# Optimization experiments

Hardware: AMD Instinct MI355X
Metric: run time of the kernel (lower is better)

The kernel has to match this reference:

```python
import jax, jax.numpy as jnp
import numpy as np

D_MODEL = 1024
H = 16
HEAD = D_MODEL // H  # 64


def setup_inputs() -> dict:
    key = jax.random.key(0)
    ks = jax.random.split(key, 10)
    B, S = 2, 2048
    x = jax.random.normal(ks[0], (B, S, D_MODEL), dtype=jnp.float32)
    y = jax.random.normal(ks[1], (B, S, D_MODEL), dtype=jnp.float32)
    mask = jnp.ones((B, S, S), dtype=jnp.float32)
    s = 1.0 / np.sqrt(D_MODEL)
    Wq = jax.random.normal(ks[2], (D_MODEL, D_MODEL), dtype=jnp.float32) * s
    Wk = jax.random.normal(ks[3], (D_MODEL, D_MODEL), dtype=jnp.float32) * s
    Wv = jax.random.normal(ks[4], (D_MODEL, D_MODEL), dtype=jnp.float32) * s
    Wo = jax.random.normal(ks[5], (D_MODEL, D_MODEL), dtype=jnp.float32) * s
    bq = jnp.zeros((D_MODEL,), jnp.float32)
    bk = jnp.zeros((D_MODEL,), jnp.float32)
    bv = jnp.zeros((D_MODEL,), jnp.float32)
    bo = jnp.zeros((D_MODEL,), jnp.float32)
    return {"x": x, "y": y, "mask": mask, "Wq": Wq, "bq": bq, "Wk": Wk,
            "bk": bk, "Wv": Wv, "bv": bv, "Wo": Wo, "bo": bo}


def reference(x, y, mask, Wq, bq, Wk, bk, Wv, bv, Wo, bo):
    # torch Linear: out = in @ W.T + b; here W stored as [out, in]
    B, Sq, D = x.shape
    Skv = y.shape[1]
    q = x @ Wq.T + bq  # [B, Sq, D]
    k = y @ Wk.T + bk  # [B, Skv, D]
    v = y @ Wv.T + bv
    # chunk(h, dim=-1) + cat(dim=0) == split feature dim into heads (head-major)
    q = q.reshape(B, Sq, H, HEAD)
    k = k.reshape(B, Skv, H, HEAD)
    v = v.reshape(B, Skv, H, HEAD)
    score = jnp.einsum('bqhd,bkhd->bhqk', q, k) / np.sqrt(HEAD)
    score = score + (1.0 - mask[:, None, :, :]) * -1e9
    attn = jax.nn.softmax(score, axis=-1)
    out = jnp.einsum('bhqk,bkhd->bqhd', attn, v).reshape(B, Sq, D)
    return out @ Wo.T + bo
```

## Files before the change

kernel.cpp:

```cpp
#include <hip/hip_runtime.h>
#include <hip/hip_bf16.h>
#include <cstdint>
#include <cstddef>

typedef __bf16 bf16x8 __attribute__((ext_vector_type(8)));
typedef float f32x4 __attribute__((ext_vector_type(4)));
typedef unsigned short u16;
typedef unsigned short u16x8 __attribute__((ext_vector_type(8)));
typedef unsigned int u32;

typedef __attribute__((address_space(1))) void gvoid_t;
typedef __attribute__((address_space(3))) void lvoid_t;

__device__ __forceinline__ void gld_lds16(const void* g, void* l) {
  __builtin_amdgcn_global_load_lds((gvoid_t*)g, (lvoid_t*)l, 16, 0, 0);
}

__device__ __forceinline__ u16 f2bf(float f) {
  u32 u = __float_as_uint(f);
  u += 0x7fffu + ((u >> 16) & 1u);
  return (u16)(u >> 16);
}
__device__ __forceinline__ u32 pack2(float a, float b) {
  __hip_bfloat162 h = __float22bfloat162_rn(float2{a, b});
  u32 r;
  __builtin_memcpy(&r, &h, 4);
  return r;
}
__device__ __forceinline__ bf16x8 ld_frag(const u16* p) {
  return __builtin_bit_cast(bf16x8, *(const uint4*)p);
}
__device__ __forceinline__ f32x4 mfma16(bf16x8 a, bf16x8 b, f32x4 c) {
  return __builtin_amdgcn_mfma_f32_16x16x32_bf16(a, b, c, 0, 0, 0);
}
__device__ __forceinline__ float ex2(float x) {
  return __builtin_amdgcn_exp2f(x);
}

#define D_MODEL 1024
#define SEQ     2048
#define NHEAD   16
#define QSC     0.1803368801f
#define MBIAS   (-1.4426950408e9f)

__global__ __launch_bounds__(256) void cvt_kernel(
    const float* __restrict__ x,  const float* __restrict__ y,
    const float* __restrict__ wq, const float* __restrict__ wk,
    const float* __restrict__ wv,
    u16* __restrict__ xb, u16* __restrict__ yb,
    u16* __restrict__ wqb, u16* __restrict__ wkb, u16* __restrict__ wvb) {
  const int t = blockIdx.y;
  const float* src;
  u16* dst;
  int n;
  float sc = 1.0f;
  if (t == 0)      { src = x;  dst = xb;  n = 4096 * 1024; }
  else if (t == 1) { src = y;  dst = yb;  n = 4096 * 1024; }
  else if (t == 2) { src = wq; dst = wqb; n = 1024 * 1024; sc = QSC; }
  else if (t == 3) { src = wk; dst = wkb; n = 1024 * 1024; }
  else             { src = wv; dst = wvb; n = 1024 * 1024; }
  const int i = (blockIdx.x * 256 + threadIdx.x) * 8;
  if (i >= n) return;
  const float4 a = *(const float4*)(src + i);
  const float4 b = *(const float4*)(src + i + 4);
  ushort4 lo, hi;
  lo.x = f2bf(a.x * sc); lo.y = f2bf(a.y * sc); lo.z = f2bf(a.z * sc); lo.w = f2bf(a.w * sc);
  hi.x = f2bf(b.x * sc); hi.y = f2bf(b.y * sc); hi.z = f2bf(b.z * sc); hi.w = f2bf(b.w * sc);
  *(ushort4*)(dst + i) = lo;
  *(ushort4*)(dst + i + 4) = hi;
}

__global__ __launch_bounds__(256) void prep_kernel(
    const float* __restrict__ mask, const float* __restrict__ wo,
    u16* __restrict__ biasC, u16* __restrict__ wob) {
  const int bid = blockIdx.x;
  if (bid < 4096) {
    const int i = (bid * 256 + threadIdx.x) * 8;
    const float4 a = *(const float4*)(mask + i);
    const float4 b = *(const float4*)(mask + i + 4);
    ushort4 lo, hi;
    lo.x = f2bf(MBIAS - a.x * MBIAS); lo.y = f2bf(MBIAS - a.y * MBIAS);
    lo.z = f2bf(MBIAS - a.z * MBIAS); lo.w = f2bf(MBIAS - a.w * MBIAS);
    hi.x = f2bf(MBIAS - b.x * MBIAS); hi.y = f2bf(MBIAS - b.y * MBIAS);
    hi.z = f2bf(MBIAS - b.z * MBIAS); hi.w = f2bf(MBIAS - b.w * MBIAS);
    *(ushort4*)(biasC + i) = lo;
    *(ushort4*)(biasC + i + 4) = hi;
  } else {
    const int i = ((bid - 4096) * 256 + threadIdx.x) * 8;
    const float4 a = *(const float4*)(wo + i);
    const float4 b = *(const float4*)(wo + i + 4);
    ushort4 lo, hi;
    lo.x = f2bf(a.x); lo.y = f2bf(a.y); lo.z = f2bf(a.z); lo.w = f2bf(a.w);
    hi.x = f2bf(b.x); hi.y = f2bf(b.y); hi.z = f2bf(b.z); hi.w = f2bf(b.w);
    *(ushort4*)(wob + i) = lo;
    *(ushort4*)(wob + i + 4) = hi;
  }
}

template <int MODE, typename OT>
__device__ __forceinline__ void gemm_block_128(const u16* __restrict__ A,
                                               const u16* __restrict__ W,
                                               const float* __restrict__ bias,
                                               float bscale,
                                               OT* __restrict__ D,
                                               int mb, int nb) {
  __shared__ __align__(16) u16 S[16384];
  u16* Asl = S;
  u16* Bsl = S + 8192;
  const int tid = threadIdx.x;
  const int w = tid >> 6, lane = tid & 63, quad = lane >> 4, l16 = lane & 15;
  const int wm = (w & 1) * 64, wn = (w >> 1) * 64;
  const int cidx = w * 64 + lane;

  f32x4 acc[4][4];
#pragma unroll
  for (int i = 0; i < 4; ++i)
#pragma unroll
    for (int j = 0; j < 4; ++j) acc[i][j] = f32x4{0.f, 0.f, 0.f, 0.f};

  for (int k0 = 0; k0 < 1024; k0 += 64) {
    __syncthreads();
#pragma unroll
    for (int t = 0; t < 4; ++t) {
      const int idx = t * 256 + cidx;
      const int row = idx >> 3;
      const int g = (idx & 7) ^ (row & 7);
      const size_t dst = (size_t)(t * 4 + w) * 1024;
      gld_lds16(A + (size_t)(mb * 128 + row) * 1024 + k0 + g * 8, (char*)Asl + dst);
      gld_lds16(W + (size_t)(nb * 128 + row) * 1024 + k0 + g * 8, (char*)Bsl + dst);
    }
    __syncthreads();

#pragma unroll
    for (int kk = 0; kk < 2; ++kk) {
      bf16x8 af[4], bfr[4];
#pragma unroll
      for (int i = 0; i < 4; ++i) {
        const int ar = wm + i * 16 + l16;
        const int br = wn + i * 16 + l16;
        af[i]  = ld_frag(Asl + ar * 64 + (((kk * 4 + quad) ^ (ar & 7)) * 8));
        bfr[i] = ld_frag(Bsl + br * 64 + (((kk * 4 + quad) ^ (br & 7)) * 8));
      }
#pragma unroll
      for (int i = 0; i < 4; ++i)
#pragma unroll
        for (int j = 0; j < 4; ++j) acc[i][j] = mfma16(af[i], bfr[j], acc[i][j]);
    }
  }

  if constexpr (MODE == 2) {
    __syncthreads();
#pragma unroll
    for (int i = 0; i < 4; ++i)
#pragma unroll
      for (int j = 0; j < 4; ++j) {
        const int dl = wn + j * 16 + l16;
        const float bv = bias[nb * 128 + dl];
        const int sx = (wm + i * 16 + quad * 4) ^ ((dl & 15) << 3);
        uint2 pv;
        pv.x = (u32)f2bf(acc[i][j][0] + bv) | ((u32)f2bf(acc[i][j][1] + bv) << 16);
        pv.y = (u32)f2bf(acc[i][j][2] + bv) | ((u32)f2bf(acc[i][j][3] + bv) << 16);
        *(uint2*)(S + dl * 128 + sx) = pv;
      }
    __syncthreads();
    const int dl = tid >> 1, half = tid & 1;
    const int bb = mb >> 4, s0 = (mb & 15) * 128;
    u16* vrow = (u16*)D + (size_t)(bb * 1024 + nb * 128 + dl) * SEQ + s0 + half * 64;
#pragma unroll
    for (int c = 0; c < 8; ++c) {
      const int pc = (half * 8 + c) ^ (dl & 15);
      *(uint4*)(vrow + c * 8) = *(const uint4*)(S + dl * 128 + pc * 8);
    }
  } else {
#pragma unroll
    for (int i = 0; i < 4; ++i)
#pragma unroll
      for (int j = 0; j < 4; ++j) {
        const int gn = nb * 128 + wn + j * 16 + l16;
        const float bv = bias[gn] * bscale;
#pragma unroll
        for (int r = 0; r < 4; ++r) {
          const int gm = mb * 128 + wm + i * 16 + quad * 4 + r;
          const float v = acc[i][j][r] + bv;
          if constexpr (sizeof(OT) == 2)
            D[(size_t)gm * 1024 + gn] = (OT)f2bf(v);
          else
            D[(size_t)gm * 1024 + gn] = (OT)v;
        }
      }
  }
}

__global__ __launch_bounds__(256) void qkv_kernel(
    const u16* __restrict__ xb, const u16* __restrict__ yb,
    const u16* __restrict__ Wqb, const u16* __restrict__ Wkb, const u16* __restrict__ Wvb,
    const float* __restrict__ bq, const float* __restrict__ bk, const float* __restrict__ bv,
    u16* __restrict__ qb, u16* __restrict__ kb, u16* __restrict__ vt) {
  const int mat = blockIdx.y >> 3;
  const int nb = blockIdx.y & 7;
  const int mb = blockIdx.x;
  if (mat == 0)      gemm_block_128<0, u16>(xb, Wqb, bq, QSC,  qb, mb, nb);
  else if (mat == 1) gemm_block_128<0, u16>(yb, Wkb, bk, 1.0f, kb, mb, nb);
  else               gemm_block_128<2, u16>(yb, Wvb, bv, 1.0f, vt, mb, nb);
}

__global__ __launch_bounds__(256) void oproj_kernel(
    const u16* __restrict__ ctx, const u16* __restrict__ Wob,
    const float* __restrict__ bo, float* __restrict__ out) {
  gemm_block_128<1, float>(ctx, Wob, bo, 1.0f, out, blockIdx.x, blockIdx.y);
}

__global__ __launch_bounds__(256) void attn_kernel(
    const u16* __restrict__ qb, const u16* __restrict__ kb,
    const u16* __restrict__ vt, const u16* __restrict__ biasC,
    u16* __restrict__ ctx) {
  const int h = blockIdx.x;
  const int qblk = blockIdx.y;
  const int b = blockIdx.z;
  const int tid = threadIdx.x, w = tid >> 6, lane = tid & 63;
  const int quad = lane >> 4, l16 = lane & 15;
  const int q0 = qblk * 128;

  __shared__ __align__(16) u16 Ks[64 * 64];
  __shared__ __align__(16) u16 Vs[64 * 64];
  __shared__ __align__(16) u16 Bs[128 * 64];
  __shared__ __align__(16) u16 Ps[4 * 32 * 64];

  const int qbase = w * 32;
  bf16x8 qf[2][2];
#pragma unroll
  for (int f = 0; f < 2; ++f) {
    const u16* qp = qb + (size_t)(b * SEQ + q0 + qbase + f * 16 + l16) * D_MODEL + h * 64;
    qf[f][0] = ld_frag(qp + quad * 8);
    qf[f][1] = ld_frag(qp + 32 + quad * 8);
  }
  bf16x8 onesf;
  {
    u16x8 t;
    const u16 ov = (l16 == 0) ? (u16)0x3F80 : (u16)0;
#pragma unroll
    for (int j = 0; j < 8; ++j) t[j] = ov;
    onesf = __builtin_bit_cast(bf16x8, t);
  }

  f32x4 O[2][4];
#pragma unroll
  for (int f = 0; f < 2; ++f)
#pragma unroll
    for (int dt = 0; dt < 4; ++dt) O[f][dt] = f32x4{0.f, 0.f, 0.f, 0.f};
  f32x4 O4[2] = {f32x4{0.f, 0.f, 0.f, 0.f}, f32x4{0.f, 0.f, 0.f, 0.f}};

  const int cidx = w * 64 + lane;
  u16* Pw = Ps + w * 2048;

  for (int kt = 0; kt < 32; ++kt) {
    const int kv0 = kt * 64;

    __syncthreads();
#pragma unroll
    for (int t = 0; t < 2; ++t) {
      const int idx = t * 256 + cidx;
      const int row = idx >> 3;
      const int g = (idx & 7) ^ (row & 7);
      const size_t dst = (size_t)(t * 4 + w) * 1024;
      gld_lds16(kb + (size_t)(b * SEQ + kv0 + row) * D_MODEL + h * 64 + g * 8,
                (char*)Ks + dst);
      gld_lds16(vt + ((size_t)((b * NHEAD + h) * 64 + row)) * SEQ + kv0 + g * 8,
                (char*)Vs + dst);
    }
#pragma unroll
    for (int t = 0; t < 4; ++t) {
      const int idx = t * 256 + cidx;
      const int row = idx >> 3;
      const int g = (idx & 7) ^ (row & 7);
      gld_lds16(biasC + (size_t)(b * SEQ + q0 + row) * SEQ + kv0 + g * 8,
                (char*)Bs + (size_t)(t * 4 + w) * 1024);
    }
    __syncthreads();

#pragma unroll
    for (int nt = 0; nt < 4; ++nt) {
      const int kvl = nt * 16 + l16;
      const bf16x8 kf0 = ld_frag(Ks + kvl * 64 + ((quad ^ (kvl & 7)) * 8));
      const bf16x8 kf1 = ld_frag(Ks + kvl * 64 + (((4 + quad) ^ (kvl & 7)) * 8));
#pragma unroll
      for (int f = 0; f < 2; ++f) {
        const int br = qbase + f * 16 + l16;
        const int ck = nt * 2 + (quad >> 1);
        const uint2 bw = *(const uint2*)(Bs + br * 64 + ((ck ^ (br & 7)) * 8) + (quad & 1) * 4);
        f32x4 z;
        z[0] = __uint_as_float(bw.x << 16);
        z[1] = __uint_as_float(bw.x & 0xffff0000u);
        z[2] = __uint_as_float(bw.y << 16);
        z[3] = __uint_as_float(bw.y & 0xffff0000u);
        z = mfma16(kf0, qf[f][0], z);
        z = mfma16(kf1, qf[f][1], z);
        uint2 pv;
        pv.x = pack2(ex2(z[0]), ex2(z[1]));
        pv.y = pack2(ex2(z[2]), ex2(z[3]));
        const int pr = f * 16 + l16;
        *(uint2*)(Pw + pr * 64 + ((ck ^ (pr & 7)) * 8) + (quad & 1) * 4) = pv;
      }
    }

    bf16x8 pf[2][2];
#pragma unroll
    for (int f = 0; f < 2; ++f) {
      const int pr = f * 16 + l16;
      pf[f][0] = ld_frag(Pw + pr * 64 + ((quad ^ (pr & 7)) * 8));
      pf[f][1] = ld_frag(Pw + pr * 64 + (((4 + quad) ^ (pr & 7)) * 8));
    }
#pragma unroll
    for (int dt = 0; dt < 4; ++dt) {
      const int vr = dt * 16 + l16;
      const bf16x8 vf0 = ld_frag(Vs + vr * 64 + ((quad ^ (vr & 7)) * 8));
      const bf16x8 vf1 = ld_frag(Vs + vr * 64 + (((4 + quad) ^ (vr & 7)) * 8));
#pragma unroll
      for (int f = 0; f < 2; ++f) {
        O[f][dt] = mfma16(pf[f][0], vf0, O[f][dt]);
        O[f][dt] = mfma16(pf[f][1], vf1, O[f][dt]);
      }
    }
#pragma unroll
    for (int f = 0; f < 2; ++f) {
      O4[f] = mfma16(pf[f][0], onesf, O4[f]);
      O4[f] = mfma16(pf[f][1], onesf, O4[f]);
    }
  }

  float inv[2][4];
#pragma unroll
  for (int f = 0; f < 2; ++f)
#pragma unroll
    for (int r = 0; r < 4; ++r)
      inv[f][r] = 1.0f / __shfl(O4[f][r], lane & 48, 64);

#pragma unroll
  for (int f = 0; f < 2; ++f)
#pragma unroll
    for (int dt = 0; dt < 4; ++dt)
#pragma unroll
      for (int r = 0; r < 4; ++r) {
        const int gq = b * SEQ + q0 + qbase + f * 16 + quad * 4 + r;
        const int gd = h * 64 + dt * 16 + l16;
        ctx[(size_t)gq * D_MODEL + gd] = f2bf(O[f][dt][r] * inv[f][r]);
      }
}

extern "C" void kernel_launch(void* const* d_in, const int* in_sizes, int n_in,
                              void* d_out, int out_size, void* d_ws, size_t ws_size,
                              hipStream_t stream) {
  (void)in_sizes; (void)n_in; (void)out_size; (void)ws_size;
  const float* x    = (const float*)d_in[0];
  const float* y    = (const float*)d_in[1];
  const float* mask = (const float*)d_in[2];
  const float* Wq   = (const float*)d_in[3];
  const float* bq   = (const float*)d_in[4];
  const float* Wk   = (const float*)d_in[5];
  const float* bk   = (const float*)d_in[6];
  const float* Wv   = (const float*)d_in[7];
  const float* bv   = (const float*)d_in[8];
  const float* Wo   = (const float*)d_in[9];
  const float* bo   = (const float*)d_in[10];
  float* out = (float*)d_out;

  const size_t M4 = (size_t)4096 * 1024;
  const size_t M1 = (size_t)1024 * 1024;
  u16* qbuf  = (u16*)d_ws;
  u16* kbuf  = qbuf + M4;
  u16* vt    = kbuf + M4;
  u16* cbuf  = vt + M4;
  u16* wob   = cbuf + M4;
  u16* xb    = wob + M1;
  u16* yb    = xb + M4;
  u16* wqb   = yb + M4;
  u16* wkb   = wqb + M1;
  u16* wvb   = wkb + M1;
  u16* biasC = xb;

  cvt_kernel<<<dim3(2048, 5, 1), 256, 0, stream>>>(x, y, Wq, Wk, Wv,
                                                   xb, yb, wqb, wkb, wvb);
  qkv_kernel<<<dim3(32, 24, 1), 256, 0, stream>>>(xb, yb, wqb, wkb, wvb,
                                                  bq, bk, bv, qbuf, kbuf, vt);
  prep_kernel<<<dim3(4608, 1, 1), 256, 0, stream>>>(mask, Wo, biasC, wob);
  attn_kernel<<<dim3(NHEAD, 16, 2), 256, 0, stream>>>(qbuf, kbuf, vt, biasC, cbuf);
  oproj_kernel<<<dim3(32, 8, 1), 256, 0, stream>>>(cbuf, wob, bo, out);
}
```

Measured before the change: 270.4 us.

## Shrink attention query tile to 64 rows and reuse bias LDS for P

The attention kernel now handles 64 query rows per block (16 per wave) instead of 128, doubling the grid to 1024 blocks. The separate score buffer in shared memory is removed: exponentiated probabilities overwrite the bias tile in place, cutting LDS use to 24 KB. The bf16 pack is replaced with a cheaper round-half-up using perm. The aim is more resident blocks and less register and LDS pressure, but K/V tiles are now loaded twice as often per query.

After: 264.5 us. -2.2%, faster.

```diff
diff --git a/kernel.cpp b/kernel.cpp
--- a/kernel.cpp
+++ b/kernel.cpp
@@ -1,5 +1,4 @@
 #include <hip/hip_runtime.h>
-#include <hip/hip_bf16.h>
 #include <cstdint>
 #include <cstddef>
 
@@ -21,11 +20,10 @@
   u += 0x7fffu + ((u >> 16) & 1u);
   return (u16)(u >> 16);
 }
-__device__ __forceinline__ u32 pack2(float a, float b) {
-  __hip_bfloat162 h = __float22bfloat162_rn(float2{a, b});
-  u32 r;
-  __builtin_memcpy(&r, &h, 4);
-  return r;
+__device__ __forceinline__ u32 pack_rnd(float a, float b) {
+  const u32 ua = __float_as_uint(a) + 0x8000u;
+  const u32 ub = __float_as_uint(b) + 0x8000u;
+  return __builtin_amdgcn_perm(ub, ua, 0x07060302u);
 }
 __device__ __forceinline__ bf16x8 ld_frag(const u16* p) {
   return __builtin_bit_cast(bf16x8, *(const uint4*)p);
@@ -219,21 +217,17 @@
   const int b = blockIdx.z;
   const int tid = threadIdx.x, w = tid >> 6, lane = tid & 63;
   const int quad = lane >> 4, l16 = lane & 15;
-  const int q0 = qblk * 128;
+  const int q0 = qblk * 64;
 
   __shared__ __align__(16) u16 Ks[64 * 64];
   __shared__ __align__(16) u16 Vs[64 * 64];
-  __shared__ __align__(16) u16 Bs[128 * 64];
-  __shared__ __align__(16) u16 Ps[4 * 32 * 64];
-
-  const int qbase = w * 32;
-  bf16x8 qf[2][2];
-#pragma unroll
-  for (int f = 0; f < 2; ++f) {
-    const u16* qp = qb + (size_t)(b * SEQ + q0 + qbase + f * 16 + l16) * D_MODEL + h * 64;
-    qf[f][0] = ld_frag(qp + quad * 8);
-    qf[f][1] = ld_frag(qp + 32 + quad * 8);
-  }
+  __shared__ __align__(16) u16 BP[64 * 64];
+
+  const int qrow = w * 16 + l16;
+  const u16* qp = qb + (size_t)(b * SEQ + q0 + qrow) * D_MODEL + h * 64;
+  const bf16x8 qf0 = ld_frag(qp + quad * 8);
+  const bf16x8 qf1 = ld_frag(qp + 32 + quad * 8);
+
   bf16x8 onesf;
   {
     u16x8 t;
@@ -243,15 +237,13 @@
     onesf = __builtin_bit_cast(bf16x8, t);
   }
 
-  f32x4 O[2][4];
-#pragma unroll
-  for (int f = 0; f < 2; ++f)
-#pragma unroll
-    for (int dt = 0; dt < 4; ++dt) O[f][dt] = f32x4{0.f, 0.f, 0.f, 0.f};
-  f32x4 O4[2] = {f32x4{0.f, 0.f, 0.f, 0.f}, f32x4{0.f, 0.f, 0.f, 0.f}};
+  f32x4 O[4];
+#pragma unroll
+  for (int dt = 0; dt < 4; ++dt) O[dt] = f32x4{0.f, 0.f, 0.f, 0.f};
+  f32x4 O4 = f32x4{0.f, 0.f, 0.f, 0.f};
 
   const int cidx = w * 64 + lane;
-  u16* Pw = Ps + w * 2048;
+  const int bhalf = (quad & 1) * 4;
 
   for (int kt = 0; kt < 32; ++kt) {
     const int kv0 = kt * 64;
@@ -267,84 +259,64 @@
                 (char*)Ks + dst);
       gld_lds16(vt + ((size_t)((b * NHEAD + h) * 64 + row)) * SEQ + kv0 + g * 8,
                 (char*)Vs + dst);
-    }
-#pragma unroll
-    for (int t = 0; t < 4; ++t) {
-      const int idx = t * 256 + cidx;
-      const int row = idx >> 3;
-      const int g = (idx & 7) ^ (row & 7);
       gld_lds16(biasC + (size_t)(b * SEQ + q0 + row) * SEQ + kv0 + g * 8,
-                (char*)Bs + (size_t)(t * 4 + w) * 1024);
-    }
-    __syncthreads();
-
+                (char*)BP + dst);
+    }
+    __syncthreads();
+
+    f32x4 z[4];
 #pragma unroll
     for (int nt = 0; nt < 4; ++nt) {
       const int kvl = nt * 16 + l16;
       const bf16x8 kf0 = ld_frag(Ks + kvl * 64 + ((quad ^ (kvl & 7)) * 8));
       const bf16x8 kf1 = ld_frag(Ks + kvl * 64 + (((4 + quad) ^ (kvl & 7)) * 8));
-#pragma unroll
-      for (int f = 0; f < 2; ++f) {
-        const int br = qbase + f * 16 + l16;
-        const int ck = nt * 2 + (quad >> 1);
-        const uint2 bw = *(const uint2*)(Bs + br * 64 + ((ck ^ (br & 7)) * 8) + (quad & 1) * 4);
-        f32x4 z;
-        z[0] = __uint_as_float(bw.x << 16);
-        z[1] = __uint_as_float(bw.x & 0xffff0000u);
-        z[2] = __uint_as_float(bw.y << 16);
-        z[3] = __uint_as_float(bw.y & 0xffff0000u);
-        z = mfma16(kf0, qf[f][0], z);
-        z = mfma16(kf1, qf[f][1], z);
-        uint2 pv;
-        pv.x = pack2(ex2(z[0]), ex2(z[1]));
-        pv.y = pack2(ex2(z[2]), ex2(z[3]));
-        const int pr = f * 16 + l16;
-        *(uint2*)(Pw + pr * 64 + ((ck ^ (pr & 7)) * 8) + (quad & 1) * 4) = pv;
-      }
-    }
-
-    bf16x8 pf[2][2];
-#pragma unroll
-    for (int f = 0; f < 2; ++f) {
-      const int pr = f * 16 + l16;
-      pf[f][0] = ld_frag(Pw + pr * 64 + ((quad ^ (pr & 7)) * 8));
-      pf[f][1] = ld_frag(Pw + pr * 64 + (((4 + quad) ^ (pr & 7)) * 8));
-    }
+      const int ck = nt * 2 + (quad >> 1);
+      const uint2 bw = *(const uint2*)(BP + qrow * 64 + ((ck ^ (qrow & 7)) * 8) + bhalf);
+      f32x4 zz;
+      zz[0] = __uint_as_float(bw.x << 16);
+      zz[1] = __uint_as_float(bw.x & 0xffff0000u);
+      zz[2] = __uint_as_float(bw.y << 16);
+      zz[3] = __uint_as_float(bw.y & 0xffff0000u);
+      zz = mfma16(kf0, qf0, zz);
+      zz = mfma16(kf1, qf1, zz);
+      z[nt] = zz;
+    }
+#pragma unroll
+    for (int nt = 0; nt < 4; ++nt) {
+      uint2 pv;
+      pv.x = pack_rnd(ex2(z[nt][0]), ex2(z[nt][1]));
+      pv.y = pack_rnd(ex2(z[nt][2]), ex2(z[nt][3]));
+      const int ck = nt * 2 + (quad >> 1);
+      *(uint2*)(BP + qrow * 64 + ((ck ^ (qrow & 7)) * 8) + bhalf) = pv;
+    }
+
+    const bf16x8 pf0 = ld_frag(BP + qrow * 64 + ((quad ^ (qrow & 7)) * 8));
+    const bf16x8 pf1 = ld_frag(BP + qrow * 64 + (((4 + quad) ^ (qrow & 7)) * 8));
 #pragma unroll
     for (int dt = 0; dt < 4; ++dt) {
       const int vr = dt * 16 + l16;
       const bf16x8 vf0 = ld_frag(Vs + vr * 64 + ((quad ^ (vr & 7)) * 8));
       const bf16x8 vf1 = ld_frag(Vs + vr * 64 + (((4 + quad) ^ (vr & 7)) * 8));
-#pragma unroll
-      for (int f = 0; f < 2; ++f) {
-        O[f][dt] = mfma16(pf[f][0], vf0, O[f][dt]);
-        O[f][dt] = mfma16(pf[f][1], vf1, O[f][dt]);
-      }
-    }
-#pragma unroll
-    for (int f = 0; f < 2; ++f) {
-      O4[f] = mfma16(pf[f][0], onesf, O4[f]);
-      O4[f] = mfma16(pf[f][1], onesf, O4[f]);
-    }
-  }
-
-  float inv[2][4];
-#pragma unroll
-  for (int f = 0; f < 2; ++f)
-#pragma unroll
-    for (int r = 0; r < 4; ++r)
-      inv[f][r] = 1.0f / __shfl(O4[f][r], lane & 48, 64);
-
-#pragma unroll
-  for (int f = 0; f < 2; ++f)
-#pragma unroll
-    for (int dt = 0; dt < 4; ++dt)
-#pragma unroll
-      for (int r = 0; r < 4; ++r) {
-        const int gq = b * SEQ + q0 + qbase + f * 16 + quad * 4 + r;
-        const int gd = h * 64 + dt * 16 + l16;
-        ctx[(size_t)gq * D_MODEL + gd] = f2bf(O[f][dt][r] * inv[f][r]);
-      }
+      O[dt] = mfma16(pf0, vf0, O[dt]);
+      O[dt] = mfma16(pf1, vf1, O[dt]);
+    }
+    O4 = mfma16(pf0, onesf, O4);
+    O4 = mfma16(pf1, onesf, O4);
+  }
+
+  float inv[4];
+#pragma unroll
+  for (int r = 0; r < 4; ++r)
+    inv[r] = 1.0f / __shfl(O4[r], lane & 48, 64);
+
+#pragma unroll
+  for (int dt = 0; dt < 4; ++dt)
+#pragma unroll
+    for (int r = 0; r < 4; ++r) {
+      const int gq = b * SEQ + q0 + w * 16 + quad * 4 + r;
+      const int gd = h * 64 + dt * 16 + l16;
+      ctx[(size_t)gq * D_MODEL + gd] = f2bf(O[dt][r] * inv[r]);
+    }
 }
 
 extern "C" void kernel_launch(void* const* d_in, const int* in_sizes, int n_in,
@@ -383,6 +355,6 @@
   qkv_kernel<<<dim3(32, 24, 1), 256, 0, stream>>>(xb, yb, wqb, wkb, wvb,
                                                   bq, bk, bv, qbuf, kbuf, vt);
   prep_kernel<<<dim3(4608, 1, 1), 256, 0, stream>>>(mask, Wo, biasC, wob);
-  attn_kernel<<<dim3(NHEAD, 16, 2), 256, 0, stream>>>(qbuf, kbuf, vt, biasC, cbuf);
+  attn_kernel<<<dim3(NHEAD, 32, 2), 256, 0, stream>>>(qbuf, kbuf, vt, biasC, cbuf);
   oproj_kernel<<<dim3(32, 8, 1), 256, 0, stream>>>(cbuf, wob, bo, out);
 }
```
